# Optimization experiments

Hardware: AMD Instinct MI355X
Metric: run time of the kernel (lower is better)

## Reference

```python
import jax, jax.numpy as jnp
import numpy as np

B, S, D = 2, 2048, 1024
H, DH = 16, 64  # num_head, head_dim; H*DH == D


def setup_inputs() -> dict:
    key = jax.random.key(0)
    ks = jax.random.split(key, 10)
    stdv = 1.0 / np.sqrt(D)
    def lin(k):
        kw, kb = jax.random.split(k)
        W = jax.random.uniform(kw, (D, D), jnp.float32, -stdv, stdv)
        b = jax.random.uniform(kb, (D,), jnp.float32, -stdv, stdv)
        return W, b
    Wq, bq = lin(ks[0]); Wk, bk = lin(ks[1]); Wv, bv = lin(ks[2]); Wo, bo = lin(ks[3])
    x = jax.random.normal(ks[4], (B, S, D), jnp.float32)
    # causal mask: True = attend
    mask = jnp.tril(jnp.ones((S, S), jnp.bool_))
    mask = jnp.broadcast_to(mask, (B, S, S))
    return {"x": x, "mask": mask, "Wq": Wq, "bq": bq, "Wk": Wk, "bk": bk,
            "Wv": Wv, "bv": bv, "Wo": Wo, "bo": bo}


def _split_head(t):
    # [B,S,D] -> [B*H, S, DH]
    return t.reshape(B, S, H, DH).transpose(0, 2, 1, 3).reshape(B * H, S, DH)


def _concat_head(t):
    # [B*H, S, DH] -> [B, S, D]
    return t.reshape(B, H, S, DH).transpose(0, 2, 1, 3).reshape(B, S, D)


def reference(x, mask, Wq, bq, Wk, bk, Wv, bv, Wo, bo):
    q = _split_head(x @ Wq.T + bq)
    k = _split_head(x @ Wk.T + bk)
    v = _split_head(x @ Wv.T + bv)
    scale = 1.0 / jnp.sqrt(jnp.float32(DH))
    # scores: [B, H, S, S], masked softmax (flash-attention math, unfused ref)
    scores = jnp.einsum('nqd,nkd->nqk', q, k).reshape(B, H, S, S) * scale
    scores = jnp.where(mask[:, None, :, :], scores, jnp.finfo(scores.dtype).min)
    attn = jax.nn.softmax(scores, axis=-1)
    out = jnp.einsum('bhqk,nkd->bhqd', attn, v.reshape(B, H, S, DH).reshape(B * H, S, DH)).reshape(B * H, S, DH) if False else jnp.einsum('nqk,nkd->nqd', attn.reshape(B * H, S, S), v)
    return _concat_head(out) @ Wo.T + bo
```

## Files before the change

kernel.cpp:

```cpp
#include <hip/hip_runtime.h>
#include <cstdint>

#define S_LEN  2048
#define NH     16
#define DHEAD  64
#define DMODEL 1024

typedef __bf16 bf16x8 __attribute__((ext_vector_type(8)));
typedef __bf16 bf16x2 __attribute__((ext_vector_type(2)));
typedef float  f32x4  __attribute__((ext_vector_type(4)));
typedef float  f32x16 __attribute__((ext_vector_type(16)));

__device__ __forceinline__ unsigned short f2bf(float x) {
  union { float f; unsigned int u; } c; c.f = x;
  unsigned int u = c.u;
  return (unsigned short)((u + 0x7fffu + ((u >> 16) & 1u)) >> 16);
}

__device__ __forceinline__ unsigned int pkbf(float a, float b) {
#if __has_builtin(__builtin_amdgcn_cvt_pk_bf16_f32)
  bf16x2 r = __builtin_amdgcn_cvt_pk_bf16_f32(a, b);
  return *(unsigned int*)&r;
#else
  return (unsigned int)f2bf(a) | ((unsigned int)f2bf(b) << 16);
#endif
}

__device__ __forceinline__ unsigned short f2bf1(float x) {
#if __has_builtin(__builtin_amdgcn_cvt_pk_bf16_f32)
  bf16x2 r = __builtin_amdgcn_cvt_pk_bf16_f32(x, x);
  union { bf16x2 v; unsigned int u; } c; c.v = r;
  return (unsigned short)(c.u & 0xffffu);
#else
  return f2bf(x);
#endif
}

__device__ __forceinline__ __bf16 us2bf(unsigned short u) {
  union { unsigned short u; __bf16 b; } c; c.u = u; return c.b;
}

__device__ __forceinline__ void glds16(const void* g, void* l) {
  __builtin_amdgcn_global_load_lds(
      (const __attribute__((address_space(1))) void*)g,
      (__attribute__((address_space(3))) void*)l, 16, 0, 0);
}

__device__ __forceinline__ f32x4 mfma16(bf16x8 a, bf16x8 b, f32x4 c) {
  return __builtin_amdgcn_mfma_f32_16x16x32_bf16(a, b, c, 0, 0, 0);
}

__device__ __forceinline__ f32x16 mfma32(bf16x8 a, bf16x8 b, f32x16 c) {
  return __builtin_amdgcn_mfma_f32_32x32x16_bf16(a, b, c, 0, 0, 0);
}

__device__ __forceinline__ void plswap(unsigned int &a, unsigned int &b) {
#if __has_builtin(__builtin_amdgcn_permlane32_swap)
  typedef unsigned int uint2v __attribute__((ext_vector_type(2)));
  uint2v r = __builtin_amdgcn_permlane32_swap(a, b, false, false);
  a = r[0]; b = r[1];
#else
  asm("v_permlane32_swap_b32 %0, %1" : "+v"(a), "+v"(b));
#endif
}

__global__ void cvt_all(const float* __restrict__ x,
                        const float* __restrict__ Wq,
                        const float* __restrict__ Wk,
                        const float* __restrict__ Wv,
                        const float* __restrict__ Wo,
                        unsigned short* __restrict__ xb,
                        unsigned short* __restrict__ wqkv,
                        unsigned short* __restrict__ wo) {
  const int b = blockIdx.x;
  const float* src;
  unsigned short* dst;
  int off;
  if (b < 4096)      { src = x;  dst = xb;                off = b; }
  else if (b < 5120) { src = Wq; dst = wqkv;              off = b - 4096; }
  else if (b < 6144) { src = Wk; dst = wqkv + (1 << 20);  off = b - 5120; }
  else if (b < 7168) { src = Wv; dst = wqkv + (2 << 20);  off = b - 6144; }
  else               { src = Wo; dst = wo;                off = b - 7168; }
  const int i = (off * 256 + threadIdx.x) * 4;
  float4 v = *(const float4*)&src[i];
  uint2 r;
  r.x = pkbf(v.x, v.y);
  r.y = pkbf(v.z, v.w);
  *(uint2*)&dst[i] = r;
}

__global__ __launch_bounds__(512, 2)
void gemm8(const unsigned short* __restrict__ A,
           const unsigned short* __restrict__ W,
           const float* __restrict__ bias0,
           const float* __restrict__ bias1,
           const float* __restrict__ bias2,
           unsigned short* __restrict__ Qt,
           unsigned short* __restrict__ Kb,
           unsigned short* __restrict__ Vt) {
  __shared__ __align__(16) unsigned short As[2][2][128 * 64];
  __shared__ __align__(16) unsigned short Bs[2][2][128 * 64];
  const int t = threadIdx.x, l = t & 63, w = t >> 6;
  const int lr = l & 15, lq = l >> 4;
  const int bid = blockIdx.x;
  const int swz = (bid & 7) * 24 + (bid >> 3);
  const int bx = swz % 12, by = swz / 12;
  const int m0 = by * 256, n0 = bx * 256;
  const int wm2 = w >> 2, wn4 = w & 3;
  const int srow = l >> 3, sslot = l & 7;

  f32x4 acc[8][4] = {};

  auto stgA = [&](int buf, int half, int kt, int j) {
    const int r  = (w + 8 * j) * 8 + srow;
    const int gs = sslot ^ (r & 7);
    glds16(A + (m0 + half * 128 + r) * 1024 + kt * 64 + gs * 8,
           &As[buf][half][r * 64 + sslot * 8]);
  };
  auto stgB = [&](int buf, int half, int kt, int j) {
    const int r  = (w + 8 * j) * 8 + srow;
    const int gs = sslot ^ (r & 7);
    glds16(W + (n0 + half * 128 + r) * 1024 + kt * 64 + gs * 8,
           &Bs[buf][half][r * 64 + sslot * 8]);
  };
  auto ldA = [&](int buf, int mi, int kk) -> bf16x8 {
    const int rr = mi * 16 + lr;
    const int sl = (kk * 4 + lq) ^ (rr & 7);
    return *(const bf16x8*)&As[buf][wm2][rr * 64 + sl * 8];
  };
  auto ldB = [&](int buf, int nj, int kk) -> bf16x8 {
    const int rr = (wn4 & 1) * 64 + nj * 16 + lr;
    const int sl = (kk * 4 + lq) ^ (rr & 7);
    return *(const bf16x8*)&Bs[buf][wn4 >> 1][rr * 64 + sl * 8];
  };

#pragma unroll
  for (int j = 0; j < 2; ++j) stgB(0, 0, 0, j);
#pragma unroll
  for (int j = 0; j < 2; ++j) stgB(0, 1, 0, j);
#pragma unroll
  for (int j = 0; j < 2; ++j) stgA(0, 0, 0, j);
#pragma unroll
  for (int j = 0; j < 2; ++j) stgA(0, 1, 0, j);
#pragma unroll
  for (int j = 0; j < 2; ++j) stgB(1, 0, 1, j);
#pragma unroll
  for (int j = 0; j < 2; ++j) stgB(1, 1, 1, j);

  const int nkt = 16;
  for (int kt = 0; kt < nkt; ++kt) {
    const int buf = kt & 1;
    if (kt + 1 < nkt) asm volatile("s_waitcnt vmcnt(4)" ::: "memory");
    else              asm volatile("s_waitcnt vmcnt(0)" ::: "memory");
    __builtin_amdgcn_s_barrier();
    __builtin_amdgcn_sched_barrier(0);

    bf16x8 bg[4][2];
#pragma unroll
    for (int nj = 0; nj < 4; ++nj) {
      bg[nj][0] = ldB(buf, nj, 0);
      bg[nj][1] = ldB(buf, nj, 1);
    }

    auto phase = [&](int q) {
      const bf16x8 a00 = ldA(buf, 2 * q, 0),     a01 = ldA(buf, 2 * q, 1);
      const bf16x8 a10 = ldA(buf, 2 * q + 1, 0), a11 = ldA(buf, 2 * q + 1, 1);
      __builtin_amdgcn_s_setprio(1);
#pragma unroll
      for (int nj = 0; nj < 4; ++nj) {
        acc[2 * q][nj]     = mfma16(a00, bg[nj][0], acc[2 * q][nj]);
        acc[2 * q][nj]     = mfma16(a01, bg[nj][1], acc[2 * q][nj]);
        acc[2 * q + 1][nj] = mfma16(a10, bg[nj][0], acc[2 * q + 1][nj]);
        acc[2 * q + 1][nj] = mfma16(a11, bg[nj][1], acc[2 * q + 1][nj]);
      }
      __builtin_amdgcn_s_setprio(0);
    };

    if (kt + 1 < nkt) { stgA(buf ^ 1, 0, kt + 1, 0); stgA(buf ^ 1, 0, kt + 1, 1); }
    phase(0);
    if (kt + 1 < nkt) { stgA(buf ^ 1, 1, kt + 1, 0); stgA(buf ^ 1, 1, kt + 1, 1); }
    phase(1);
    __builtin_amdgcn_s_barrier();
    __builtin_amdgcn_sched_barrier(0);
    if (kt + 2 < nkt) { stgB(buf, 0, kt + 2, 0); stgB(buf, 0, kt + 2, 1); }
    phase(2);
    if (kt + 2 < nkt) { stgB(buf, 1, kt + 2, 0); stgB(buf, 1, kt + 2, 1); }
    phase(3);
  }

  const int tsel = n0 >> 10;
#pragma unroll
  for (int mi = 0; mi < 8; ++mi) {
#pragma unroll
    for (int nj = 0; nj < 4; ++nj) {
      const int mb = m0 + wm2 * 128 + mi * 16 + lq * 4;
      const int n  = n0 + wn4 * 64 + nj * 16 + lr;
      const int d  = n & 1023;
      const int bidx = mb >> 11, s = mb & (S_LEN - 1);
      const int h = d >> 6, dh = d & 63;
      const int bh = bidx * NH + h;
      const float bv0 = (tsel == 0) ? bias0[d] : ((tsel == 1) ? bias1[d] : bias2[d]);
      if (tsel == 0) {
        const float sc = 0.125f * 1.44269504088896f;
#pragma unroll
        for (int r = 0; r < 4; ++r)
          Qt[(bh * S_LEN + s + r) * DHEAD + dh] = f2bf1((acc[mi][nj][r] + bv0) * sc);
      } else if (tsel == 2) {
        uint2 pv;
        pv.x = pkbf(acc[mi][nj][0] + bv0, acc[mi][nj][1] + bv0);
        pv.y = pkbf(acc[mi][nj][2] + bv0, acc[mi][nj][3] + bv0);
        *(uint2*)&Vt[(bh * DHEAD + dh) * S_LEN + s] = pv;
      } else {
#pragma unroll
        for (int r = 0; r < 4; ++r)
          Kb[(bh * S_LEN + s + r) * DHEAD + dh] = f2bf1(acc[mi][nj][r] + bv0);
      }
    }
  }
}

template<int MODE, int BN>
__global__ __launch_bounds__(256)
void gemm_bt(const unsigned short* __restrict__ A,
             const unsigned short* __restrict__ W,
             const float* __restrict__ bias0,
             float* __restrict__ Out,
             int K) {
  constexpr int JN = BN / 32;
  __shared__ __align__(16) unsigned short As[2][128 * 32];
  __shared__ __align__(16) unsigned short Bs[2][BN * 32];
  const int t    = threadIdx.x;
  const int lane = t & 63;
  const int w    = t >> 6;
  const int lr   = lane & 15, lq = lane >> 4;
  const int wm   = (w >> 1) * 64, wn = (w & 1) * (BN / 2);
  const int m0   = blockIdx.y * 128, n0 = blockIdx.x * BN;
  const int ra   = t >> 2, ca = (t & 3) * 8;

  f32x4 acc[4][JN] = {};

  const int niter = K >> 6;
  for (int kk = 0; kk < niter; ++kk) {
    const int k0 = kk << 6;
#pragma unroll
    for (int kh = 0; kh < 2; ++kh) {
      const int kc = k0 + kh * 32;
      glds16(A + (m0 + ra) * K + kc + ca,      &As[kh][ra * 32 + ca]);
      glds16(A + (m0 + 64 + ra) * K + kc + ca, &As[kh][(64 + ra) * 32 + ca]);
      glds16(W + (n0 + ra) * K + kc + ca,      &Bs[kh][ra * 32 + ca]);
      if (BN == 128)
        glds16(W + (n0 + 64 + ra) * K + kc + ca, &Bs[kh][(64 + ra) * 32 + ca]);
    }
    __syncthreads();
#pragma unroll
    for (int kh = 0; kh < 2; ++kh) {
      bf16x8 af[4], bg[JN];
#pragma unroll
      for (int i = 0; i < 4; ++i)
        af[i] = *(const bf16x8*)&As[kh][(wm + i * 16 + lr) * 32 + lq * 8];
#pragma unroll
      for (int j = 0; j < JN; ++j)
        bg[j] = *(const bf16x8*)&Bs[kh][(wn + j * 16 + lr) * 32 + lq * 8];
#pragma unroll
      for (int i = 0; i < 4; ++i)
#pragma unroll
        for (int j = 0; j < JN; ++j)
          acc[i][j] = mfma16(af[i], bg[j], acc[i][j]);
    }
    __syncthreads();
  }

#pragma unroll
  for (int i = 0; i < 4; ++i)
#pragma unroll
    for (int j = 0; j < JN; ++j)
#pragma unroll
      for (int r = 0; r < 4; ++r) {
        const int m = m0 + wm + i * 16 + lq * 4 + r;
        const int n = n0 + wn + j * 16 + lr;
        Out[m * DMODEL + n] = acc[i][j][r] + bias0[n];
      }
}

__global__ __launch_bounds__(256, 2)
void flash_kernel(const unsigned short* __restrict__ Qt,
                  const unsigned short* __restrict__ Kb,
                  const unsigned short* __restrict__ Vt,
                  unsigned short* __restrict__ Ocat) {
  __shared__ __align__(16) unsigned short Ks[2][2][64 * 64];
  __shared__ __align__(16) unsigned short Vs[2][2][64 * 64];
  __shared__ float MlS[2][32];
  const int w = threadIdx.x >> 6, lane = threadIdx.x & 63;
  const int l31 = lane & 31, half = lane >> 5;
  const int qh = w & 1, sub = w >> 1;
  const int bh = blockIdx.x;
  const int pp = blockIdx.y;
  const char* Kc = (const char*)(Kb + bh * (S_LEN * DHEAD));
  const char* Vc = (const char*)(Vt + bh * (DHEAD * S_LEN));
  const unsigned short* Qp = Qt + bh * (S_LEN * DHEAD);
  const int bb = bh >> 4, hd = bh & 15;

  bf16x8 ones;
#pragma unroll
  for (int j = 0; j < 8; ++j) ones[j] = (__bf16)1.0f;

  auto run_strip = [&](int sb) {
    const int len = sb + 1;
    const int nit = (len + 1) >> 1;
    const int q0 = sb * 64;
    const int qa = q0 + qh * 32 + l31;
    bf16x8 qf[4];
#pragma unroll
    for (int d = 0; d < 4; ++d)
      qf[d] = *(const bf16x8*)&Qp[qa * 64 + d * 16 + half * 8];
    f32x16 o0 = {}, o1 = {}, lacc = {};

    auto stage = [&](int buf, int it) {
#pragma unroll
      for (int s2 = 0; s2 < 2; ++s2) {
        const int kt = 2 * it + s2;
#pragma unroll
        for (int h8 = 0; h8 < 2; ++h8) {
          const int rb = w * 16 + h8 * 8;
          const int r  = rb + (lane >> 3);
          const int gs = (lane & 7) ^ (r & 7) ^ ((r >> 3) & 3);
          glds16(Kc + (kt * 64 + r) * 128 + gs * 16, &Ks[buf][s2][rb * 64]);
          glds16(Vc + r * 4096 + kt * 128 + gs * 16, &Vs[buf][s2][rb * 64]);
        }
      }
    };

    stage(0, 0);
    for (int it = 0; it < nit; ++it) {
      const int buf = it & 1;
      __syncthreads();
      if (it + 1 < nit) stage(1 - buf, it + 1);
      const int kt = 2 * it + sub;
      if (kt < len) {
        const unsigned short* Kt = &Ks[buf][sub][0];
        const unsigned short* Vl = &Vs[buf][sub][0];
        const int r0 = l31, r1 = 32 + l31;
        const int x0 = (r0 & 7) ^ ((r0 >> 3) & 3);
        const int x1 = (r1 & 7) ^ ((r1 >> 3) & 3);
        f32x16 st0 = {}, st1 = {};
#pragma unroll
        for (int d = 0; d < 4; ++d) {
          const int sl = d * 2 + half;
          st0 = mfma32(*(const bf16x8*)&Kt[r0 * 64 + ((sl ^ x0) << 3)], qf[d], st0);
          st1 = mfma32(*(const bf16x8*)&Kt[r1 * 64 + ((sl ^ x1) << 3)], qf[d], st1);
        }
        const bool diag = (kt == sb);
        unsigned int pk0[8], pk1[8];
#pragma unroll
        for (int m = 0; m < 8; ++m) {
          const int rA = 2 * m, rB = 2 * m + 1;
          const int kA = (rA & 3) + 8 * (rA >> 2) + 4 * half;
          const int kB = (rB & 3) + 8 * (rB >> 2) + 4 * half;
          float e0 = __builtin_amdgcn_exp2f(st0[rA]);
          float e1 = __builtin_amdgcn_exp2f(st0[rB]);
          float f0 = __builtin_amdgcn_exp2f(st1[rA]);
          float f1 = __builtin_amdgcn_exp2f(st1[rB]);
          if (diag) {
            e0 = (kt * 64 + kA > qa) ? 0.f : e0;
            e1 = (kt * 64 + kB > qa) ? 0.f : e1;
            f0 = (kt * 64 + 32 + kA > qa) ? 0.f : f0;
            f1 = (kt * 64 + 32 + kB > qa) ? 0.f : f1;
          }
          pk0[m] = pkbf(e0, e1);
          pk1[m] = pkbf(f0, f1);
        }
#pragma unroll
        for (int s = 0; s < 4; ++s) {
          unsigned int u, u2, v, v2;
          if (s == 0)      { u = pk0[0]; u2 = pk0[1]; v = pk0[2]; v2 = pk0[3]; }
          else if (s == 1) { u = pk0[4]; u2 = pk0[5]; v = pk0[6]; v2 = pk0[7]; }
          else if (s == 2) { u = pk1[0]; u2 = pk1[1]; v = pk1[2]; v2 = pk1[3]; }
          else             { u = pk1[4]; u2 = pk1[5]; v = pk1[6]; v2 = pk1[7]; }
          plswap(u, v);
          plswap(u2, v2);
          union { unsigned int ui[4]; bf16x8 bv; } pf;
          pf.ui[0] = u; pf.ui[1] = u2; pf.ui[2] = v; pf.ui[3] = v2;
          const int sl = s * 2 + half;
          o0 = mfma32(*(const bf16x8*)&Vl[r0 * 64 + ((sl ^ x0) << 3)], pf.bv, o0);
          o1 = mfma32(*(const bf16x8*)&Vl[r1 * 64 + ((sl ^ x1) << 3)], pf.bv, o1);
          lacc = mfma32(ones, pf.bv, lacc);
        }
      }
    }

    float* Mo = (float*)&Ks[1 - ((nit - 1) & 1)][0][0];
    const int qrow = qh * 32 + l31;
    if (sub == 1) {
      if (lane < 32) MlS[qh][l31] = lacc[0];
#pragma unroll
      for (int g = 0; g < 4; ++g) {
        const int sl0 = 2 * g + half;
        const int sl1 = 8 + 2 * g + half;
        f32x4 s0 = { o0[4 * g], o0[4 * g + 1], o0[4 * g + 2], o0[4 * g + 3] };
        f32x4 s1 = { o1[4 * g], o1[4 * g + 1], o1[4 * g + 2], o1[4 * g + 3] };
        *(f32x4*)&Mo[qrow * 64 + ((sl0 ^ (qrow & 15)) << 2)] = s0;
        *(f32x4*)&Mo[qrow * 64 + ((sl1 ^ (qrow & 15)) << 2)] = s1;
      }
    }
    __syncthreads();
    if (sub == 0) {
      const float inv = 1.f / (lacc[0] + MlS[qh][l31]);
      unsigned short* Or = Ocat + (bb * S_LEN + q0 + qrow) * DMODEL + hd * DHEAD;
#pragma unroll
      for (int g = 0; g < 4; ++g) {
        const int sl0 = 2 * g + half;
        const int sl1 = 8 + 2 * g + half;
        const f32x4 m0 = *(const f32x4*)&Mo[qrow * 64 + ((sl0 ^ (qrow & 15)) << 2)];
        const f32x4 m1 = *(const f32x4*)&Mo[qrow * 64 + ((sl1 ^ (qrow & 15)) << 2)];
        uint2 ov0, ov1;
        ov0.x = pkbf((o0[4 * g]     + m0[0]) * inv, (o0[4 * g + 1] + m0[1]) * inv);
        ov0.y = pkbf((o0[4 * g + 2] + m0[2]) * inv, (o0[4 * g + 3] + m0[3]) * inv);
        ov1.x = pkbf((o1[4 * g]     + m1[0]) * inv, (o1[4 * g + 1] + m1[1]) * inv);
        ov1.y = pkbf((o1[4 * g + 2] + m1[2]) * inv, (o1[4 * g + 3] + m1[3]) * inv);
        *(uint2*)&Or[8 * g + 4 * half]      = ov0;
        *(uint2*)&Or[32 + 8 * g + 4 * half] = ov1;
      }
    }
    __syncthreads();
  };

  run_strip(31 - pp);
  run_strip(pp);
}

extern "C" void kernel_launch(void* const* d_in, const int* in_sizes, int n_in,
                              void* d_out, int out_size, void* d_ws, size_t ws_size,
                              hipStream_t stream) {
  const float* x  = (const float*)d_in[0];
  const float* Wq = (const float*)d_in[2];
  const float* bq = (const float*)d_in[3];
  const float* Wk = (const float*)d_in[4];
  const float* bk = (const float*)d_in[5];
  const float* Wv = (const float*)d_in[6];
  const float* bv = (const float*)d_in[7];
  const float* Wo = (const float*)d_in[8];
  const float* bo = (const float*)d_in[9];
  float* out = (float*)d_out;

  char* ws = (char*)d_ws;
  unsigned short* xb   = (unsigned short*)(ws);
  unsigned short* wqkv = (unsigned short*)(ws + (8ull  << 20));
  unsigned short* wo   = (unsigned short*)(ws + (14ull << 20));
  unsigned short* Qt   = (unsigned short*)(ws + (16ull << 20));
  unsigned short* Kb   = (unsigned short*)(ws + (24ull << 20));
  unsigned short* Vt   = (unsigned short*)(ws + (32ull << 20));
  unsigned short* Ocat = (unsigned short*)(ws + (40ull << 20));

  cvt_all<<<8192, 256, 0, stream>>>(x, Wq, Wk, Wv, Wo, xb, wqkv, wo);

  gemm8<<<192, 512, 0, stream>>>(xb, wqkv, bq, bk, bv, Qt, Kb, Vt);
  flash_kernel<<<dim3(32, 16), 256, 0, stream>>>(Qt, Kb, Vt, Ocat);
  gemm_bt<1, 64><<<dim3(16, 32), 256, 0, stream>>>(Ocat, wo, bo, out, 1024);
}
```

Baseline: 210.9 us.

## Restructure QKV GEMM pipeline barriers and swizzle LDS in output GEMM

```diff
diff --git a/kernel.cpp b/kernel.cpp
--- a/kernel.cpp
+++ b/kernel.cpp
@@ -89,7 +89,7 @@
   *(uint2*)&dst[i] = r;
 }
 
-__global__ __launch_bounds__(512, 2)
+__global__ __launch_bounds__(512)
 void gemm8(const unsigned short* __restrict__ A,
            const unsigned short* __restrict__ W,
            const float* __restrict__ bias0,
@@ -111,17 +111,23 @@
 
   f32x4 acc[8][4] = {};
 
-  auto stgA = [&](int buf, int half, int kt, int j) {
-    const int r  = (w + 8 * j) * 8 + srow;
-    const int gs = sslot ^ (r & 7);
-    glds16(A + (m0 + half * 128 + r) * 1024 + kt * 64 + gs * 8,
-           &As[buf][half][r * 64 + sslot * 8]);
+  auto stgA = [&](int buf, int half, int kt) {
+#pragma unroll
+    for (int j = 0; j < 2; ++j) {
+      const int r  = (w + 8 * j) * 8 + srow;
+      const int gs = sslot ^ (r & 7);
+      glds16(A + (m0 + half * 128 + r) * 1024 + kt * 64 + gs * 8,
+             &As[buf][half][r * 64 + sslot * 8]);
+    }
   };
-  auto stgB = [&](int buf, int half, int kt, int j) {
-    const int r  = (w + 8 * j) * 8 + srow;
-    const int gs = sslot ^ (r & 7);
-    glds16(W + (n0 + half * 128 + r) * 1024 + kt * 64 + gs * 8,
-           &Bs[buf][half][r * 64 + sslot * 8]);
+  auto stgB = [&](int buf, int half, int kt) {
+#pragma unroll
+    for (int j = 0; j < 2; ++j) {
+      const int r  = (w + 8 * j) * 8 + srow;
+      const int gs = sslot ^ (r & 7);
+      glds16(W + (n0 + half * 128 + r) * 1024 + kt * 64 + gs * 8,
+             &Bs[buf][half][r * 64 + sslot * 8]);
+    }
   };
   auto ldA = [&](int buf, int mi, int kk) -> bf16x8 {
     const int rr = mi * 16 + lr;
@@ -134,58 +140,98 @@
     return *(const bf16x8*)&Bs[buf][wn4 >> 1][rr * 64 + sl * 8];
   };
 
-#pragma unroll
-  for (int j = 0; j < 2; ++j) stgB(0, 0, 0, j);
-#pragma unroll
-  for (int j = 0; j < 2; ++j) stgB(0, 1, 0, j);
-#pragma unroll
-  for (int j = 0; j < 2; ++j) stgA(0, 0, 0, j);
-#pragma unroll
-  for (int j = 0; j < 2; ++j) stgA(0, 1, 0, j);
-#pragma unroll
-  for (int j = 0; j < 2; ++j) stgB(1, 0, 1, j);
-#pragma unroll
-  for (int j = 0; j < 2; ++j) stgB(1, 1, 1, j);
+  stgB(0, 0, 0); stgB(0, 1, 0);
+  stgA(0, 0, 0); stgA(0, 1, 0);
+  stgB(1, 0, 1); stgB(1, 1, 1);
+  asm volatile("s_waitcnt vmcnt(4)" ::: "memory");
+  __builtin_amdgcn_s_barrier();
 
   const int nkt = 16;
-  for (int kt = 0; kt < nkt; ++kt) {
-    const int buf = kt & 1;
-    if (kt + 1 < nkt) asm volatile("s_waitcnt vmcnt(4)" ::: "memory");
-    else              asm volatile("s_waitcnt vmcnt(0)" ::: "memory");
-    __builtin_amdgcn_s_barrier();
-    __builtin_amdgcn_sched_barrier(0);
-
+  for (int U = 0; U < nkt; ++U) {
+    const int bc = U & 1;
     bf16x8 bg[4][2];
+
 #pragma unroll
     for (int nj = 0; nj < 4; ++nj) {
-      bg[nj][0] = ldB(buf, nj, 0);
-      bg[nj][1] = ldB(buf, nj, 1);
-    }
-
-    auto phase = [&](int q) {
-      const bf16x8 a00 = ldA(buf, 2 * q, 0),     a01 = ldA(buf, 2 * q, 1);
-      const bf16x8 a10 = ldA(buf, 2 * q + 1, 0), a11 = ldA(buf, 2 * q + 1, 1);
+      bg[nj][0] = ldB(bc, nj, 0);
+      bg[nj][1] = ldB(bc, nj, 1);
+    }
+    {
+      bf16x8 a0 = ldA(bc, 0, 0), a1 = ldA(bc, 0, 1);
+      bf16x8 a2 = ldA(bc, 1, 0), a3 = ldA(bc, 1, 1);
+      if (U + 1 < nkt) stgA(1 - bc, 0, U + 1);
+      __builtin_amdgcn_s_barrier();
+      asm volatile("s_waitcnt lgkmcnt(0)" ::: "memory");
+      __builtin_amdgcn_sched_barrier(0);
       __builtin_amdgcn_s_setprio(1);
 #pragma unroll
       for (int nj = 0; nj < 4; ++nj) {
-        acc[2 * q][nj]     = mfma16(a00, bg[nj][0], acc[2 * q][nj]);
-        acc[2 * q][nj]     = mfma16(a01, bg[nj][1], acc[2 * q][nj]);
-        acc[2 * q + 1][nj] = mfma16(a10, bg[nj][0], acc[2 * q + 1][nj]);
-        acc[2 * q + 1][nj] = mfma16(a11, bg[nj][1], acc[2 * q + 1][nj]);
+        acc[0][nj] = mfma16(a0, bg[nj][0], acc[0][nj]);
+        acc[0][nj] = mfma16(a1, bg[nj][1], acc[0][nj]);
+        acc[1][nj] = mfma16(a2, bg[nj][0], acc[1][nj]);
+        acc[1][nj] = mfma16(a3, bg[nj][1], acc[1][nj]);
       }
       __builtin_amdgcn_s_setprio(0);
-    };
-
-    if (kt + 1 < nkt) { stgA(buf ^ 1, 0, kt + 1, 0); stgA(buf ^ 1, 0, kt + 1, 1); }
-    phase(0);
-    if (kt + 1 < nkt) { stgA(buf ^ 1, 1, kt + 1, 0); stgA(buf ^ 1, 1, kt + 1, 1); }
-    phase(1);
-    __builtin_amdgcn_s_barrier();
-    __builtin_amdgcn_sched_barrier(0);
-    if (kt + 2 < nkt) { stgB(buf, 0, kt + 2, 0); stgB(buf, 0, kt + 2, 1); }
-    phase(2);
-    if (kt + 2 < nkt) { stgB(buf, 1, kt + 2, 0); stgB(buf, 1, kt + 2, 1); }
-    phase(3);
+      __builtin_amdgcn_s_barrier();
+    }
+    {
+      bf16x8 a0 = ldA(bc, 2, 0), a1 = ldA(bc, 2, 1);
+      bf16x8 a2 = ldA(bc, 3, 0), a3 = ldA(bc, 3, 1);
+      if (U + 1 < nkt) stgA(1 - bc, 1, U + 1);
+      __builtin_amdgcn_s_barrier();
+      asm volatile("s_waitcnt lgkmcnt(0)" ::: "memory");
+      __builtin_amdgcn_sched_barrier(0);
+      __builtin_amdgcn_s_setprio(1);
+#pragma unroll
+      for (int nj = 0; nj < 4; ++nj) {
+        acc[2][nj] = mfma16(a0, bg[nj][0], acc[2][nj]);
+        acc[2][nj] = mfma16(a1, bg[nj][1], acc[2][nj]);
+        acc[3][nj] = mfma16(a2, bg[nj][0], acc[3][nj]);
+        acc[3][nj] = mfma16(a3, bg[nj][1], acc[3][nj]);
+      }
+      __builtin_amdgcn_s_setprio(0);
+      __builtin_amdgcn_s_barrier();
+    }
+    {
+      bf16x8 a0 = ldA(bc, 4, 0), a1 = ldA(bc, 4, 1);
+      bf16x8 a2 = ldA(bc, 5, 0), a3 = ldA(bc, 5, 1);
+      if (U + 2 < nkt) stgB(bc, 0, U + 2);
+      __builtin_amdgcn_s_barrier();
+      asm volatile("s_waitcnt lgkmcnt(0)" ::: "memory");
+      __builtin_amdgcn_sched_barrier(0);
+      __builtin_amdgcn_s_setprio(1);
+#pragma unroll
+      for (int nj = 0; nj < 4; ++nj) {
+        acc[4][nj] = mfma16(a0, bg[nj][0], acc[4][nj]);
+        acc[4][nj] = mfma16(a1, bg[nj][1], acc[4][nj]);
+        acc[5][nj] = mfma16(a2, bg[nj][0], acc[5][nj]);
+        acc[5][nj] = mfma16(a3, bg[nj][1], acc[5][nj]);
+      }
+      __builtin_amdgcn_s_setprio(0);
+      __builtin_amdgcn_s_barrier();
+    }
+    {
+      bf16x8 a0 = ldA(bc, 6, 0), a1 = ldA(bc, 6, 1);
+      bf16x8 a2 = ldA(bc, 7, 0), a3 = ldA(bc, 7, 1);
+      if (U + 2 < nkt) stgB(bc, 1, U + 2);
+      __builtin_amdgcn_s_barrier();
+      asm volatile("s_waitcnt lgkmcnt(0)" ::: "memory");
+      __builtin_amdgcn_sched_barrier(0);
+      __builtin_amdgcn_s_setprio(1);
+#pragma unroll
+      for (int nj = 0; nj < 4; ++nj) {
+        acc[6][nj] = mfma16(a0, bg[nj][0], acc[6][nj]);
+        acc[6][nj] = mfma16(a1, bg[nj][1], acc[6][nj]);
+        acc[7][nj] = mfma16(a2, bg[nj][0], acc[7][nj]);
+        acc[7][nj] = mfma16(a3, bg[nj][1], acc[7][nj]);
+      }
+      __builtin_amdgcn_s_setprio(0);
+      if (U + 1 < nkt) {
+        if (U + 1 == nkt - 1) asm volatile("s_waitcnt vmcnt(0)" ::: "memory");
+        else                  asm volatile("s_waitcnt vmcnt(4)" ::: "memory");
+      }
+      __builtin_amdgcn_s_barrier();
+    }
   }
 
   const int tsel = n0 >> 10;
@@ -235,7 +281,10 @@
   const int lr   = lane & 15, lq = lane >> 4;
   const int wm   = (w >> 1) * 64, wn = (w & 1) * (BN / 2);
   const int m0   = blockIdx.y * 128, n0 = blockIdx.x * BN;
-  const int ra   = t >> 2, ca = (t & 3) * 8;
+  const int ra   = t >> 2, cs = t & 3;
+  const int gca  = (cs ^ ((ra >> 1) & 3)) * 8;
+  const int lca  = cs * 8;
+  const int xsw  = (lr >> 1) & 3;
 
   f32x4 acc[4][JN] = {};
 
@@ -245,11 +294,11 @@
 #pragma unroll
     for (int kh = 0; kh < 2; ++kh) {
       const int kc = k0 + kh * 32;
-      glds16(A + (m0 + ra) * K + kc + ca,      &As[kh][ra * 32 + ca]);
-      glds16(A + (m0 + 64 + ra) * K + kc + ca, &As[kh][(64 + ra) * 32 + ca]);
-      glds16(W + (n0 + ra) * K + kc + ca,      &Bs[kh][ra * 32 + ca]);
+      glds16(A + (m0 + ra) * K + kc + gca,      &As[kh][ra * 32 + lca]);
+      glds16(A + (m0 + 64 + ra) * K + kc + gca, &As[kh][(64 + ra) * 32 + lca]);
+      glds16(W + (n0 + ra) * K + kc + gca,      &Bs[kh][ra * 32 + lca]);
       if (BN == 128)
-        glds16(W + (n0 + 64 + ra) * K + kc + ca, &Bs[kh][(64 + ra) * 32 + ca]);
+        glds16(W + (n0 + 64 + ra) * K + kc + gca, &Bs[kh][(64 + ra) * 32 + lca]);
     }
     __syncthreads();
 #pragma unroll
@@ -257,10 +306,10 @@
       bf16x8 af[4], bg[JN];
 #pragma unroll
       for (int i = 0; i < 4; ++i)
-        af[i] = *(const bf16x8*)&As[kh][(wm + i * 16 + lr) * 32 + lq * 8];
+        af[i] = *(const bf16x8*)&As[kh][(wm + i * 16 + lr) * 32 + ((lq ^ xsw) * 8)];
 #pragma unroll
       for (int j = 0; j < JN; ++j)
-        bg[j] = *(const bf16x8*)&Bs[kh][(wn + j * 16 + lr) * 32 + lq * 8];
+        bg[j] = *(const bf16x8*)&Bs[kh][(wn + j * 16 + lr) * 32 + ((lq ^ xsw) * 8)];
 #pragma unroll
       for (int i = 0; i < 4; ++i)
 #pragma unroll
```

New measurement: 206.4 us. 1.02x faster.
